# Optimization experiments

Measured on AMD Instinct MI355X. Metric: run time of the kernel, lower is better.

Reference implementation:

```python
import jax, jax.numpy as jnp
from jax import lax
import numpy as np

B, N, C = 32, 24564, 81
CENTER_VAR, SIZE_VAR = 0.1, 0.2
CONF_THRESH, IOU_THRESH = 0.01, 0.45
PRE_NMS_K, MAX_DET = 100, 100
EPS = 1e-8


def setup_inputs() -> dict:
    key = jax.random.key(0)
    k1, k2, k3, k4 = jax.random.split(key, 4)
    location_preds = jax.random.normal(k1, (B, N, 4), dtype=jnp.float32)
    confidence_preds = jax.random.normal(k2, (B, N, C), dtype=jnp.float32)
    # priors in center form (cx, cy, w, h), all in (0, 1), w/h in [0.05, 0.5]
    cxcy = jax.random.uniform(k3, (N, 2), dtype=jnp.float32)
    wh = 0.05 + 0.45 * jax.random.uniform(k4, (N, 2), dtype=jnp.float32)
    priors = jnp.concatenate([cxcy, wh], axis=-1)
    return {"location_preds": location_preds,
            "confidence_preds": confidence_preds,
            "priors": priors}


def _decode_corner(loc, priors):
    # loc: [B,N,4], priors: [N,4] center form -> corner-form boxes [B,N,4]
    cxcy = loc[..., :2] * CENTER_VAR * priors[None, :, 2:] + priors[None, :, :2]
    wh = jnp.exp(loc[..., 2:] * SIZE_VAR) * priors[None, :, 2:]
    return jnp.concatenate([cxcy - wh * 0.5, cxcy + wh * 0.5], axis=-1)


def _pairwise_iou(boxes):
    # boxes: [K,4] corner form -> [K,K]
    lt = jnp.maximum(boxes[:, None, :2], boxes[None, :, :2])
    rb = jnp.minimum(boxes[:, None, 2:], boxes[None, :, 2:])
    wh = jnp.clip(rb - lt, 0.0)
    inter = wh[..., 0] * wh[..., 1]
    area = jnp.prod(jnp.clip(boxes[:, 2:] - boxes[:, :2], 0.0), axis=-1)  # [K]
    return inter / (area[:, None] + area[None, :] - inter + EPS)


def _nms_one_class(boxes, scores):
    # boxes: [N,4], scores: [N] -> kept top-K boxes/scores for this class
    scores = jnp.where(scores > CONF_THRESH, scores, 0.0)
    top_s, idx = lax.top_k(scores, PRE_NMS_K)          # [K]
    top_b = boxes[idx]                                  # [K,4] sorted by score desc
    iou = _pairwise_iou(top_b)                          # [K,K]
    order = jnp.arange(PRE_NMS_K)

    def body(i, keep):
        suppressed = jnp.any(keep & (iou[:, i] > IOU_THRESH) & (order < i))
        return keep.at[i].set((top_s[i] > 0.0) & jnp.logical_not(suppressed))

    keep = lax.fori_loop(0, PRE_NMS_K, body, jnp.zeros(PRE_NMS_K, dtype=bool))
    return top_b, jnp.where(keep, top_s, 0.0)


def _per_image(boxes, scores):
    # boxes: [N,4], scores: [N,C]; class 0 is background
    cls_scores = scores[:, 1:].T                        # [C-1, N]
    b, s = jax.vmap(_nms_one_class, in_axes=(None, 0))(boxes, cls_scores)
    labels = jnp.broadcast_to(jnp.arange(1, C)[:, None], (C - 1, PRE_NMS_K))
    b = b.reshape(-1, 4)
    s = s.reshape(-1)
    labels = labels.reshape(-1)
    top_s, idx = lax.top_k(s, MAX_DET)
    return b[idx], top_s, labels[idx]


def reference(location_preds, confidence_preds, priors):
    scores = jax.nn.softmax(confidence_preds, axis=2)   # [B,N,C]
    bboxes = _decode_corner(location_preds, priors)     # [B,N,4]
    boxes_out, scores_out, labels_out = jax.vmap(_per_image)(bboxes, scores)
    # boxes_out [B,MAX_DET,4], scores_out [B,MAX_DET], labels_out [B,MAX_DET]
    return boxes_out, scores_out, labels_out
```

## Files before the change

kernel.cpp:

```cpp
#include <hip/hip_runtime.h>
#include <cstdint>
#include <cstddef>

#define BB 32
#define NN 24564
#define CC 81
#define CM1 80
#define KTOP 100
#define MAXDET 100
#define CBINS 28
#define CSHIFT 21
#define BASEBITS 0x3C000000u
#define SPECBITS 0x3D400000u
#define SPECPF   0.0468281f
#define CAP2 2048
#define CAPB 25
#define BPI 96
#define CAPS 1024
#define FCH 8
#define FCHN 1000
#define FPAD 1024

typedef unsigned long long ull;
typedef unsigned int uint;
typedef float floatx4 __attribute__((ext_vector_type(4)));
typedef floatx4 uf4 __attribute__((aligned(4)));

__global__ __launch_bounds__(256) void zero_kernel(uint* __restrict__ p, int nwords) {
    int i = blockIdx.x * 256 + threadIdx.x;
    if (i < nwords) p[i] = 0u;
}

__global__ __launch_bounds__(256) void softmax_spec_kernel(const float* __restrict__ conf,
                                                           float2* __restrict__ mxs,
                                                           ull* __restrict__ cand,
                                                           uint* __restrict__ ccnt,
                                                           uint* __restrict__ ovf) {
    __shared__ ull  sbuf[CM1 * CAPB];
    __shared__ uint scnt[CM1];
    int tid = threadIdx.x;
    if (tid < CM1) scnt[tid] = 0u;
    __syncthreads();

    int b = blockIdx.x / BPI, j = blockIdx.x % BPI;
    int n = j * 256 + tid;
    if (n < NN) {
        const float* row = conf + ((size_t)b * NN + n) * CC;
        const uf4* row4 = reinterpret_cast<const uf4*>(row);
        float r[CC];
        #pragma unroll
        for (int q = 0; q < 20; ++q) {
            floatx4 v = row4[q];
            r[4 * q] = v.x; r[4 * q + 1] = v.y; r[4 * q + 2] = v.z; r[4 * q + 3] = v.w;
        }
        r[80] = row[80];

        float mx = r[0];
        #pragma unroll
        for (int c = 1; c < CC; ++c) mx = fmaxf(mx, r[c]);

        float s = 0.f;
        #pragma unroll
        for (int c = 0; c < CC; ++c) {
            r[c] = expf(__fsub_rn(r[c], mx));
            s = __fadd_rn(s, r[c]);
        }
        mxs[(size_t)b * NN + n] = make_float2(mx, s);

        float rcp = __builtin_amdgcn_rcpf(s);
        uint nn = (uint)n;
        #pragma unroll
        for (int c = 1; c < CC; ++c) {
            float p = __fmul_rn(r[c], rcp);
            if (p > SPECPF) {
                float sc = __fdiv_rn(r[c], s);
                uint eb = __float_as_uint(sc);
                if (eb >= SPECBITS) {
                    uint pp = atomicAdd(&scnt[c - 1], 1u);
                    if (pp < CAPB) sbuf[(c - 1) * CAPB + pp] = (((ull)(~eb)) << 32) | nn;
                }
            }
        }
    }
    __syncthreads();

    if (tid < CM1) {
        uint c2 = scnt[tid];
        if (c2) {
            int bc = b * CM1 + tid;
            uint nstore = c2 > CAPB ? CAPB : c2;
            uint base = atomicAdd(ccnt + bc, nstore);
            if (c2 > CAPB || base + nstore > CAP2) ovf[bc] = 1u;
            uint lim = base + nstore; if (lim > CAP2) lim = CAP2;
            for (uint i = 0; base + i < lim; ++i)
                cand[(size_t)bc * CAP2 + base + i] = sbuf[tid * CAPB + i];
        }
    }
}

__global__ __launch_bounds__(256) void nms_kernel(const ull* __restrict__ cand,
                                                  const uint* __restrict__ ccnt,
                                                  const uint* __restrict__ ovf,
                                                  const float* __restrict__ conf,
                                                  const float2* __restrict__ mxs,
                                                  const float* __restrict__ loc,
                                                  const float* __restrict__ priors,
                                                  float* __restrict__ nms_scores,
                                                  float* __restrict__ nms_boxes) {
    int bc = blockIdx.x;
    int bimg = bc / CM1, ccls = bc % CM1;
    __shared__ ull arr[CAP2];
    __shared__ ull arr2[CAPS];
    __shared__ uint hist[CBINS];
    __shared__ uint s_cut, s_mode, s_cnt2;
    __shared__ float bx[KTOP][4];
    __shared__ float sv[KTOP];
    __shared__ ull mlo[KTOP], mhi[KTOP];
    __shared__ ull keeplo, keephi;

    int tid = threadIdx.x;
    for (int i = tid; i < CBINS; i += 256) hist[i] = 0u;
    if (tid == 0) { s_cut = 0u; s_mode = 0u; s_cnt2 = 0u; }
    __syncthreads();

    uint rawcnt = ccnt[bc];
    bool flagged = !(ovf[bc] == 0u && rawcnt >= (uint)KTOP);
    int scc; ull* sorted;

    if (!flagged) {
        int cc = (int)rawcnt; if (cc > CAP2) cc = CAP2;
        const ull* crow = cand + (size_t)bc * CAP2;
        for (int i = tid; i < cc; i += 256) {
            ull k = crow[i];
            arr[i] = k;
            uint bits = ~(uint)(k >> 32);
            uint bin = (bits - BASEBITS) >> CSHIFT;
            if (bin >= CBINS) bin = CBINS - 1;
            atomicAdd(&hist[bin], 1u);
        }
        __syncthreads();
        if (tid == 0) {
            uint Kt = (uint)(cc < KTOP ? cc : KTOP);
            if (Kt > 0) {
                uint cum = 0; int bb2 = 0;
                for (int i = CBINS - 1; i >= 0; --i) {
                    cum += hist[i];
                    if (cum >= Kt) { bb2 = i; break; }
                }
                if (cum <= CAPS) {
                    s_cut = BASEBITS + ((uint)bb2 << CSHIFT);
                    s_mode = 1u;
                }
            }
        }
        __syncthreads();
        if (s_mode) {
            uint cutv = s_cut;
            for (int i = tid; i < cc; i += 256) {
                ull k = arr[i];
                uint bits = ~(uint)(k >> 32);
                if (bits >= cutv) { uint p = atomicAdd(&s_cnt2, 1u); arr2[p] = k; }
            }
            __syncthreads();
            scc = (int)s_cnt2;
            sorted = arr2;
        } else {
            scc = cc;
            sorted = arr;
        }
    } else {
        int c = ccls + 1;
        for (int n = tid; n < NN; n += 256) {
            float x = conf[((size_t)bimg * NN + n) * CC + c];
            float2 ms = mxs[(size_t)bimg * NN + n];
            float e = expf(__fsub_rn(x, ms.x));
            float sc = __fdiv_rn(e, ms.y);
            if (sc > 0.01f) {
                uint bits = __float_as_uint(sc);
                uint bin = (bits - BASEBITS) >> CSHIFT;
                if (bin >= CBINS) bin = CBINS - 1;
                atomicAdd(&hist[bin], 1u);
            }
        }
        __syncthreads();
        if (tid == 0) {
            uint total = 0;
            for (int i = 0; i < CBINS; ++i) total += hist[i];
            uint Kt = total < KTOP ? total : KTOP;
            s_cut = 0xFFFFFFFFu;
            if (Kt > 0) {
                uint cum = 0; int bb2 = 0;
                for (int i = CBINS - 1; i >= 0; --i) {
                    cum += hist[i];
                    if (cum >= Kt) { bb2 = i; break; }
                }
                uint cutbin = (cum <= CAP2) ? (uint)bb2 : (uint)(bb2 + 1);
                s_cut = BASEBITS + (cutbin << CSHIFT);
            }
        }
        __syncthreads();
        uint cutv = s_cut;
        for (int n = tid; n < NN; n += 256) {
            float x = conf[((size_t)bimg * NN + n) * CC + c];
            float2 ms = mxs[(size_t)bimg * NN + n];
            float e = expf(__fsub_rn(x, ms.x));
            float sc = __fdiv_rn(e, ms.y);
            if (sc > 0.01f) {
                uint bits = __float_as_uint(sc);
                if (bits >= cutv) {
                    uint p = atomicAdd(&s_cnt2, 1u);
                    if (p < CAP2) arr[p] = (((ull)(~bits)) << 32) | (uint)n;
                }
            }
        }
        __syncthreads();
        scc = (int)s_cnt2; if (scc > CAP2) scc = CAP2;
        sorted = arr;
    }

    int S = 1; while (S < scc) S <<= 1; if (S < 2) S = 2;
    for (int i = scc + tid; i < S; i += 256) sorted[i] = ~0ull;
    __syncthreads();

    for (int k = 2; k <= S; k <<= 1) {
        for (int jj = k >> 1; jj > 0; jj >>= 1) {
            for (int i = tid; i < S; i += 256) {
                int ixj = i ^ jj;
                if (ixj > i) {
                    ull a = sorted[i], b2 = sorted[ixj];
                    bool up = ((i & k) == 0);
                    if ((a > b2) == up) { sorted[i] = b2; sorted[ixj] = a; }
                }
            }
            __syncthreads();
        }
    }

    if (tid < KTOP) {
        float val = 0.f; uint n = 0;
        if (tid < scc) {
            ull kk = sorted[tid];
            val = __uint_as_float(~(uint)(kk >> 32));
            n = (uint)(kk & 0xFFFFFFFFu);
        }
        sv[tid] = val;
        float4 l = reinterpret_cast<const float4*>(loc)[(size_t)bimg * NN + n];
        float4 p = reinterpret_cast<const float4*>(priors)[n];
        float cx = __fadd_rn(__fmul_rn(__fmul_rn(l.x, 0.1f), p.z), p.x);
        float cy = __fadd_rn(__fmul_rn(__fmul_rn(l.y, 0.1f), p.w), p.y);
        float w  = __fmul_rn(expf(__fmul_rn(l.z, 0.2f)), p.z);
        float h  = __fmul_rn(expf(__fmul_rn(l.w, 0.2f)), p.w);
        bx[tid][0] = __fsub_rn(cx, __fmul_rn(w, 0.5f));
        bx[tid][1] = __fsub_rn(cy, __fmul_rn(h, 0.5f));
        bx[tid][2] = __fadd_rn(cx, __fmul_rn(w, 0.5f));
        bx[tid][3] = __fadd_rn(cy, __fmul_rn(h, 0.5f));
    }
    __syncthreads();

    if (tid < KTOP) {
        float x1 = bx[tid][0], y1 = bx[tid][1], x2 = bx[tid][2], y2 = bx[tid][3];
        float ai = __fmul_rn(fmaxf(__fsub_rn(x2, x1), 0.f), fmaxf(__fsub_rn(y2, y1), 0.f));
        ull lo = 0, hi = 0;
        for (int jj = 0; jj < KTOP; ++jj) {
            float jx1 = bx[jj][0], jy1 = bx[jj][1], jx2 = bx[jj][2], jy2 = bx[jj][3];
            float iw = fmaxf(__fsub_rn(fminf(x2, jx2), fmaxf(x1, jx1)), 0.f);
            float ih = fmaxf(__fsub_rn(fminf(y2, jy2), fmaxf(y1, jy1)), 0.f);
            float inter = __fmul_rn(iw, ih);
            float aj = __fmul_rn(fmaxf(__fsub_rn(jx2, jx1), 0.f), fmaxf(__fsub_rn(jy2, jy1), 0.f));
            float denom = __fadd_rn(__fsub_rn(__fadd_rn(ai, aj), inter), 1e-8f);
            float iou = __fdiv_rn(inter, denom);
            if (iou > 0.45f) { if (jj < 64) lo |= (1ull << jj); else hi |= (1ull << (jj - 64)); }
        }
        mlo[tid] = lo; mhi[tid] = hi;
    }
    __syncthreads();

    if (tid == 0) {
        ull klo = 0, khi = 0;
        for (int i = 0; i < KTOP; ++i) {
            ull sup = (mlo[i] & klo) | (mhi[i] & khi);
            bool kp = (sv[i] > 0.f) && (sup == 0ull);
            if (kp) { if (i < 64) klo |= (1ull << i); else khi |= (1ull << (i - 64)); }
        }
        keeplo = klo; keephi = khi;
    }
    __syncthreads();

    if (tid < KTOP) {
        bool kp = (tid < 64) ? ((keeplo >> tid) & 1ull) : ((keephi >> (tid - 64)) & 1ull);
        size_t obase = (size_t)bc * KTOP + tid;
        nms_scores[obase] = kp ? sv[tid] : 0.f;
        float4 o; o.x = bx[tid][0]; o.y = bx[tid][1]; o.z = bx[tid][2]; o.w = bx[tid][3];
        reinterpret_cast<float4*>(nms_boxes)[obase] = o;
    }
}

__global__ __launch_bounds__(256) void final_partial_kernel(const float* __restrict__ nms_scores,
                                                            ull* __restrict__ fkeys) {
    int blk = blockIdx.x;
    int b = blk / FCH, ch = blk % FCH;
    __shared__ ull arr[FPAD];
    int tid = threadIdx.x;
    const float* srow = nms_scores + (size_t)b * (CM1 * KTOP) + ch * FCHN;
    for (int i = tid; i < FPAD; i += 256) {
        ull key;
        if (i < FCHN) {
            float s = srow[i];
            uint bits = (s > 0.f) ? __float_as_uint(s) : 0u;
            key = (((ull)(~bits)) << 32) | (uint)(ch * FCHN + i);
        } else key = ~0ull;
        arr[i] = key;
    }
    __syncthreads();
    for (int k = 2; k <= FPAD; k <<= 1) {
        for (int jj = k >> 1; jj > 0; jj >>= 1) {
            for (int i = tid; i < FPAD; i += 256) {
                int ixj = i ^ jj;
                if (ixj > i) {
                    ull a = arr[i], b2 = arr[ixj];
                    bool up = ((i & k) == 0);
                    if ((a > b2) == up) { arr[i] = b2; arr[ixj] = a; }
                }
            }
            __syncthreads();
        }
    }
    if (tid < KTOP)
        fkeys[(size_t)b * (FCH * KTOP) + ch * KTOP + tid] = arr[tid];
}

__global__ __launch_bounds__(256) void final_merge_kernel(const ull* __restrict__ fkeys,
                                                          const float* __restrict__ nms_boxes,
                                                          float* __restrict__ out) {
    int b = blockIdx.x;
    __shared__ ull arr[FPAD];
    int tid = threadIdx.x;
    const ull* krow = fkeys + (size_t)b * (FCH * KTOP);
    for (int i = tid; i < FPAD; i += 256)
        arr[i] = (i < FCH * KTOP) ? krow[i] : ~0ull;
    __syncthreads();
    for (int k = 2; k <= FPAD; k <<= 1) {
        for (int jj = k >> 1; jj > 0; jj >>= 1) {
            for (int i = tid; i < FPAD; i += 256) {
                int ixj = i ^ jj;
                if (ixj > i) {
                    ull a = arr[i], b2 = arr[ixj];
                    bool up = ((i & k) == 0);
                    if ((a > b2) == up) { arr[i] = b2; arr[ixj] = a; }
                }
            }
            __syncthreads();
        }
    }
    if (tid < MAXDET) {
        ull kk = arr[tid];
        uint hb = (uint)(kk >> 32);
        uint idx = (uint)(kk & 0xFFFFFFFFu);
        float val = __uint_as_float(~hb);
        float4 b4 = reinterpret_cast<const float4*>(nms_boxes)[(size_t)b * (CM1 * KTOP) + idx];
        reinterpret_cast<float4*>(out)[(size_t)b * MAXDET + tid] = b4;
        out[BB * MAXDET * 4 + b * MAXDET + tid] = val;
        out[BB * MAXDET * 5 + b * MAXDET + tid] = (float)(idx / KTOP + 1);
    }
}

extern "C" void kernel_launch(void* const* d_in, const int* in_sizes, int n_in,
                              void* d_out, int out_size, void* d_ws, size_t ws_size,
                              hipStream_t stream) {
    const float* loc    = (const float*)d_in[0];
    const float* conf   = (const float*)d_in[1];
    const float* priors = (const float*)d_in[2];
    float* out = (float*)d_out;

    char* ws = (char*)d_ws;
    float* nms_scores = (float*)ws;
    float* nms_boxes  = nms_scores + (size_t)BB * CM1 * KTOP;
    ull*   cand       = (ull*)(nms_boxes + (size_t)BB * CM1 * KTOP * 4);
    float2* mxs       = (float2*)(cand + (size_t)BB * CM1 * CAP2);
    ull*   fkeys      = (ull*)(mxs + (size_t)BB * NN);
    uint*  ccnt       = (uint*)(fkeys + (size_t)BB * FCH * KTOP);
    uint*  ovf        = ccnt + (size_t)BB * CM1;

    zero_kernel<<<(BB * CM1 * 2 + 255) / 256, 256, 0, stream>>>(ccnt, BB * CM1 * 2);

    softmax_spec_kernel<<<BB * BPI, 256, 0, stream>>>(conf, mxs, cand, ccnt, ovf);
    nms_kernel<<<BB * CM1, 256, 0, stream>>>(cand, ccnt, ovf, conf, mxs, loc, priors,
                                             nms_scores, nms_boxes);
    final_partial_kernel<<<BB * FCH, 256, 0, stream>>>(nms_scores, fkeys);
    final_merge_kernel<<<BB, 256, 0, stream>>>(fkeys, nms_boxes, out);
}
```

Measured before the change: 270.1 us.

## Fuse final top-k into NMS kernel via last-block-per-image atomic counter

Removes the two final sort kernels and instead has the last NMS block finishing for each image (detected with a per-image atomic counter and threadfence) perform the final top-100 selection. That selection uses a histogram-based threshold on the score bits so only candidates above a cutoff are sorted, and it falls back to the chunked bitonic sorts if the cutoff does not apply. The goal is to save two kernel launches and the full 8000-element sorts. In exchange, the final work is serialized onto one block per image at the tail of the NMS grid.

Result: slower. 429.6 us (+59.1%).

```diff
diff --git a/kernel.cpp b/kernel.cpp
--- a/kernel.cpp
+++ b/kernel.cpp
@@ -20,6 +20,7 @@
 #define FCH 8
 #define FCHN 1000
 #define FPAD 1024
+#define NCAND (CM1 * KTOP)
 
 typedef unsigned long long ull;
 typedef unsigned int uint;
@@ -29,6 +30,22 @@
 __global__ __launch_bounds__(256) void zero_kernel(uint* __restrict__ p, int nwords) {
     int i = blockIdx.x * 256 + threadIdx.x;
     if (i < nwords) p[i] = 0u;
+}
+
+__device__ __forceinline__ void bitonic_sort256(ull* a, int S, int tid) {
+    for (int k = 2; k <= S; k <<= 1) {
+        for (int j = k >> 1; j > 0; j >>= 1) {
+            for (int i = tid; i < S; i += 256) {
+                int ixj = i ^ j;
+                if (ixj > i) {
+                    ull x = a[i], y = a[ixj];
+                    bool up = ((i & k) == 0);
+                    if ((x > y) == up) { a[i] = y; a[ixj] = x; }
+                }
+            }
+            __syncthreads();
+        }
+    }
 }
 
 __global__ __launch_bounds__(256) void softmax_spec_kernel(const float* __restrict__ conf,
@@ -106,13 +123,15 @@
                                                   const float* __restrict__ loc,
                                                   const float* __restrict__ priors,
                                                   float* __restrict__ nms_scores,
-                                                  float* __restrict__ nms_boxes) {
+                                                  float* __restrict__ nms_boxes,
+                                                  uint* __restrict__ done,
+                                                  float* __restrict__ out) {
     int bc = blockIdx.x;
     int bimg = bc / CM1, ccls = bc % CM1;
     __shared__ ull arr[CAP2];
     __shared__ ull arr2[CAPS];
     __shared__ uint hist[CBINS];
-    __shared__ uint s_cut, s_mode, s_cnt2;
+    __shared__ uint s_cut, s_mode, s_cnt2, s_nz, s_last;
     __shared__ float bx[KTOP][4];
     __shared__ float sv[KTOP];
     __shared__ ull mlo[KTOP], mhi[KTOP];
@@ -221,20 +240,7 @@
     int S = 1; while (S < scc) S <<= 1; if (S < 2) S = 2;
     for (int i = scc + tid; i < S; i += 256) sorted[i] = ~0ull;
     __syncthreads();
-
-    for (int k = 2; k <= S; k <<= 1) {
-        for (int jj = k >> 1; jj > 0; jj >>= 1) {
-            for (int i = tid; i < S; i += 256) {
-                int ixj = i ^ jj;
-                if (ixj > i) {
-                    ull a = sorted[i], b2 = sorted[ixj];
-                    bool up = ((i & k) == 0);
-                    if ((a > b2) == up) { sorted[i] = b2; sorted[ixj] = a; }
-                }
-            }
-            __syncthreads();
-        }
-    }
+    bitonic_sort256(sorted, S, tid);
 
     if (tid < KTOP) {
         float val = 0.f; uint n = 0;
@@ -293,74 +299,95 @@
         float4 o; o.x = bx[tid][0]; o.y = bx[tid][1]; o.z = bx[tid][2]; o.w = bx[tid][3];
         reinterpret_cast<float4*>(nms_boxes)[obase] = o;
     }
-}
-
-__global__ __launch_bounds__(256) void final_partial_kernel(const float* __restrict__ nms_scores,
-                                                            ull* __restrict__ fkeys) {
-    int blk = blockIdx.x;
-    int b = blk / FCH, ch = blk % FCH;
-    __shared__ ull arr[FPAD];
-    int tid = threadIdx.x;
-    const float* srow = nms_scores + (size_t)b * (CM1 * KTOP) + ch * FCHN;
-    for (int i = tid; i < FPAD; i += 256) {
-        ull key;
-        if (i < FCHN) {
+
+    __threadfence();
+    __syncthreads();
+    if (tid == 0) {
+        uint prev = atomicAdd(&done[bimg], 1u);
+        s_last = (prev == (uint)(CM1 - 1)) ? 1u : 0u;
+    }
+    __syncthreads();
+    if (!s_last) return;
+    __threadfence();
+
+    const float* srow = nms_scores + (size_t)bimg * NCAND;
+    for (int i = tid; i < CBINS; i += 256) hist[i] = 0u;
+    if (tid == 0) { s_cut = 0u; s_mode = 0u; s_cnt2 = 0u; s_nz = 0u; }
+    __syncthreads();
+
+    uint mynz = 0;
+    for (int i = tid; i < NCAND; i += 256) {
+        float s = srow[i];
+        if (s > 0.f) {
+            ++mynz;
+            uint bits = __float_as_uint(s);
+            uint bin = (bits - BASEBITS) >> CSHIFT;
+            if (bin >= CBINS) bin = CBINS - 1;
+            atomicAdd(&hist[bin], 1u);
+        }
+    }
+    if (mynz) atomicAdd(&s_nz, mynz);
+    __syncthreads();
+    if (tid == 0) {
+        if (s_nz >= (uint)KTOP) {
+            uint cum = 0; int bb2 = 0;
+            for (int i = CBINS - 1; i >= 0; --i) {
+                cum += hist[i];
+                if (cum >= (uint)KTOP) { bb2 = i; break; }
+            }
+            if (cum <= CAP2) { s_cut = BASEBITS + ((uint)bb2 << CSHIFT); s_mode = 1u; }
+        }
+    }
+    __syncthreads();
+
+    if (s_mode) {
+        uint cutv = s_cut;
+        for (int i = tid; i < NCAND; i += 256) {
             float s = srow[i];
-            uint bits = (s > 0.f) ? __float_as_uint(s) : 0u;
-            key = (((ull)(~bits)) << 32) | (uint)(ch * FCHN + i);
-        } else key = ~0ull;
-        arr[i] = key;
-    }
-    __syncthreads();
-    for (int k = 2; k <= FPAD; k <<= 1) {
-        for (int jj = k >> 1; jj > 0; jj >>= 1) {
+            if (s > 0.f) {
+                uint bits = __float_as_uint(s);
+                if (bits >= cutv) {
+                    uint p = atomicAdd(&s_cnt2, 1u);
+                    arr[p] = (((ull)(~bits)) << 32) | (uint)i;
+                }
+            }
+        }
+        __syncthreads();
+        int fcc = (int)s_cnt2;
+        int FS = 1; while (FS < fcc) FS <<= 1; if (FS < 2) FS = 2;
+        for (int i = fcc + tid; i < FS; i += 256) arr[i] = ~0ull;
+        __syncthreads();
+        bitonic_sort256(arr, FS, tid);
+    } else {
+        for (int ch = 0; ch < FCH; ++ch) {
             for (int i = tid; i < FPAD; i += 256) {
-                int ixj = i ^ jj;
-                if (ixj > i) {
-                    ull a = arr[i], b2 = arr[ixj];
-                    bool up = ((i & k) == 0);
-                    if ((a > b2) == up) { arr[i] = b2; arr[ixj] = a; }
-                }
+                ull key;
+                if (i < FCHN) {
+                    float s = srow[ch * FCHN + i];
+                    uint bits = (s > 0.f) ? __float_as_uint(s) : 0u;
+                    key = (((ull)(~bits)) << 32) | (uint)(ch * FCHN + i);
+                } else key = ~0ull;
+                arr2[i] = key;
             }
             __syncthreads();
-        }
-    }
-    if (tid < KTOP)
-        fkeys[(size_t)b * (FCH * KTOP) + ch * KTOP + tid] = arr[tid];
-}
-
-__global__ __launch_bounds__(256) void final_merge_kernel(const ull* __restrict__ fkeys,
-                                                          const float* __restrict__ nms_boxes,
-                                                          float* __restrict__ out) {
-    int b = blockIdx.x;
-    __shared__ ull arr[FPAD];
-    int tid = threadIdx.x;
-    const ull* krow = fkeys + (size_t)b * (FCH * KTOP);
-    for (int i = tid; i < FPAD; i += 256)
-        arr[i] = (i < FCH * KTOP) ? krow[i] : ~0ull;
-    __syncthreads();
-    for (int k = 2; k <= FPAD; k <<= 1) {
-        for (int jj = k >> 1; jj > 0; jj >>= 1) {
-            for (int i = tid; i < FPAD; i += 256) {
-                int ixj = i ^ jj;
-                if (ixj > i) {
-                    ull a = arr[i], b2 = arr[ixj];
-                    bool up = ((i & k) == 0);
-                    if ((a > b2) == up) { arr[i] = b2; arr[ixj] = a; }
-                }
-            }
+            bitonic_sort256(arr2, FPAD, tid);
+            if (tid < KTOP) arr[ch * KTOP + tid] = arr2[tid];
             __syncthreads();
         }
-    }
+        for (int i = FCH * KTOP + tid; i < FPAD; i += 256) arr[i] = ~0ull;
+        __syncthreads();
+        bitonic_sort256(arr, FPAD, tid);
+    }
+
     if (tid < MAXDET) {
         ull kk = arr[tid];
         uint hb = (uint)(kk >> 32);
         uint idx = (uint)(kk & 0xFFFFFFFFu);
         float val = __uint_as_float(~hb);
-        float4 b4 = reinterpret_cast<const float4*>(nms_boxes)[(size_t)b * (CM1 * KTOP) + idx];
-        reinterpret_cast<float4*>(out)[(size_t)b * MAXDET + tid] = b4;
-        out[BB * MAXDET * 4 + b * MAXDET + tid] = val;
-        out[BB * MAXDET * 5 + b * MAXDET + tid] = (float)(idx / KTOP + 1);
+        float4 b4 = reinterpret_cast<const float4*>(nms_boxes)[(size_t)bimg * NCAND + idx];
+        reinterpret_cast<float4*>(out)[(size_t)bimg * MAXDET + tid] = b4;
+        out[BB * MAXDET * 4 + bimg * MAXDET + tid] = val;
+        out[BB * MAXDET * 5 + bimg * MAXDET + tid] = (float)(idx / KTOP + 1);
     }
 }
 
@@ -377,15 +404,14 @@
     float* nms_boxes  = nms_scores + (size_t)BB * CM1 * KTOP;
     ull*   cand       = (ull*)(nms_boxes + (size_t)BB * CM1 * KTOP * 4);
     float2* mxs       = (float2*)(cand + (size_t)BB * CM1 * CAP2);
-    ull*   fkeys      = (ull*)(mxs + (size_t)BB * NN);
-    uint*  ccnt       = (uint*)(fkeys + (size_t)BB * FCH * KTOP);
+    uint*  ccnt       = (uint*)(mxs + (size_t)BB * NN);
     uint*  ovf        = ccnt + (size_t)BB * CM1;
-
-    zero_kernel<<<(BB * CM1 * 2 + 255) / 256, 256, 0, stream>>>(ccnt, BB * CM1 * 2);
+    uint*  done       = ovf + (size_t)BB * CM1;
+
+    const int zwords = BB * CM1 * 2 + BB;
+    zero_kernel<<<(zwords + 255) / 256, 256, 0, stream>>>(ccnt, zwords);
 
     softmax_spec_kernel<<<BB * BPI, 256, 0, stream>>>(conf, mxs, cand, ccnt, ovf);
     nms_kernel<<<BB * CM1, 256, 0, stream>>>(cand, ccnt, ovf, conf, mxs, loc, priors,
-                                             nms_scores, nms_boxes);
-    final_partial_kernel<<<BB * FCH, 256, 0, stream>>>(nms_scores, fkeys);
-    final_merge_kernel<<<BB, 256, 0, stream>>>(fkeys, nms_boxes, out);
+                                             nms_scores, nms_boxes, done, out);
 }
```
